# Optimization experiments

Hardware: AMD Instinct MI355X
Metric: run time of the kernel (lower is better)

Reference implementation:

```python
import jax, jax.numpy as jnp
import numpy as np

H = 128   # hidden_size
NL = 3    # num_layers
R = 32    # water_rows (Water2sea_slice_num)
O = 48    # water_cols (Original_slice_len)
B = 64    # batch_size
F = 32    # input_size
L = R + O - 1  # Water2sea_slice_len (wavefront length)


def setup_inputs():
    key = jax.random.key(0)
    k1, k2, k3, k4 = jax.random.split(key, 4)
    stdv = 1.0 / np.sqrt(H)
    inp = jax.random.normal(k1, (B, R, O, F), dtype=jnp.float32)
    W_first = jax.random.uniform(k2, (6 * H, F + 2 * H), minval=-stdv, maxval=stdv, dtype=jnp.float32)
    W_other = jax.random.uniform(k3, (NL - 1, 6 * H, 4 * H), minval=-stdv, maxval=stdv, dtype=jnp.float32)
    Bias = jax.random.uniform(k4, (NL, 6 * H), minval=-stdv, maxval=stdv, dtype=jnp.float32)
    return {"input": inp, "W_first": W_first, "W_other": W_other, "Bias": Bias,
            "batch_size": B, "input_size": F, "flag": 0}


def _forward(inp, W_first, W_other, Bias, batch_size, input_size, flag):
    # permute: flag==0 -> [rows, batch, cols, feat]
    x = jnp.transpose(inp, (2, 0, 1, 3)) if flag == 1 else jnp.transpose(inp, (1, 0, 2, 3))
    Rn, bs, On, Fn = x.shape
    Ln = Rn + On - 1
    # wavefront-shifted input: row r occupies slices [r, r+On) (input_transfer)
    padded = jnp.pad(x, ((0, 0), (0, 0), (0, Rn - 1), (0, 0)))                 # [R,B,L,F]
    shifted = jax.vmap(lambda t, r: jnp.roll(t, r, axis=1))(padded, jnp.arange(Rn))
    a0 = shifted.reshape(Rn * bs, Ln, Fn)
    # bias applied to row-group g at slice s iff (s < Rn) and (g <= s)  [faithful to linear()]
    s_idx = jnp.arange(Ln)[:, None]
    g_idx = jnp.arange(Rn)[None, :]
    bias_mask = ((g_idx <= s_idx) & (s_idx < Rn)).astype(jnp.float32)          # [L,R]
    bias_mask = jnp.repeat(bias_mask, bs, axis=1)[..., None]                   # [L,RB,1]

    def run_layer(a, W, bvec):
        # a: [RB, L, feat]; W: [6H, feat+2H]; bvec: [6H]
        def step(carry, xs):
            h_row, h_col = carry
            a_s, m_s = xs
            z = jnp.concatenate([h_row, h_col, a_s], axis=-1)
            gate = z @ W.T + m_s * bvec                                        # [RB,6H]
            sig = jax.nn.sigmoid(gate[:, :4 * H])
            tnh = jnp.tanh(gate[:, 4 * H:])
            ur, orow, uc, ocol = jnp.split(sig, 4, axis=-1)
            ir, ic = jnp.split(tnh, 2, axis=-1)
            h_row_n = jnp.tanh((1.0 - ur) * h_row + ur * ir) * orow
            h_col_n = jnp.tanh((1.0 - uc) * h_col + uc * ic) * ocol
            out = jnp.concatenate([h_row_n, h_col_n], axis=-1)
            h_col_roll = jnp.roll(h_col_n, bs, axis=0)  # transfer col hidden to next row
            return (h_row_n, h_col_roll), (out, h_row_n, h_col_n)
        h0 = jnp.zeros((Rn * bs, H), a.dtype)
        _, (outs, hrows, hcols) = jax.lax.scan(step, (h0, h0), (jnp.swapaxes(a, 0, 1), bias_mask))
        return outs, hrows, hcols  # each [L, RB, *]

    row_saves, col_saves = [], []
    a = a0
    for layer in range(NL):
        W = W_first if layer == 0 else W_other[layer - 1]
        outs, hrows, hcols = run_layer(a, W, Bias[layer])
        hrows = hrows.reshape(Ln, Rn, bs, H)
        hcols = hcols.reshape(Ln, Rn, bs, H)
        # row r finishes at slice On-1+r; col hidden of last row-group saved for slices >= Rn-1
        row_saves.append(hrows[On - 1 + jnp.arange(Rn), jnp.arange(Rn)])       # [R,B,H]
        col_saves.append(hcols[Rn - 1:, Rn - 1])                               # [O,B,H]
        a = jnp.swapaxes(outs, 0, 1)                                           # [RB,L,2H]; dropout p=0 -> identity
    output_all_slice = a
    hidden_row_all = jnp.transpose(jnp.stack(row_saves), (2, 0, 1, 3))         # [B,NL,R,H]
    hidden_col_all = jnp.transpose(jnp.stack(col_saves), (2, 0, 1, 3))         # [B,NL,O,H]
    return output_all_slice, hidden_row_all, hidden_col_all


def reference(input, W_first, W_other, Bias, batch_size, input_size, flag):
    return _forward(input, W_first, W_other, Bias, batch_size, input_size, flag)
```

## Files before the change

### kernel.cpp

```cpp
#include <hip/hip_runtime.h>
#include <stdint.h>

#define HH   128
#define NLAY 3
#define RR   32
#define OO   48
#define BBX  64
#define FFX  32
#define LLX  (RR + OO - 1)
#define RBr  (RR * BBX)
#define N6   (6 * HH)
#define TSTEPS (LLX + NLAY - 1)
#define NBLOCKS 192

typedef unsigned short u16;
typedef __attribute__((ext_vector_type(8))) short short8;
typedef __attribute__((ext_vector_type(4))) float f32x4;

#define OFF_ABUF0 ((size_t)0)
#define SZ_ABUF0  ((size_t)LLX * RBr * FFX * 2)
#define OFF_HZ    (OFF_ABUF0 + SZ_ABUF0)
#define SZ_HZ     ((size_t)NLAY * 2 * RBr * 256 * 2)
#define OFF_BAR   (OFF_HZ + SZ_HZ)
#define SZ_BAR    ((size_t)32768)
#define SZ_STATE  (SZ_HZ + SZ_BAR)

__device__ __forceinline__ u16 f2b(float x) {
  uint32_t u = __float_as_uint(x);
  return (u16)((u + 0x7FFFu + ((u >> 16) & 1u)) >> 16);
}
__device__ __forceinline__ float rcp_(float x) { return __builtin_amdgcn_rcpf(x); }
__device__ __forceinline__ float sigmoidf_(float x) {
  return rcp_(1.0f + __expf(-x));
}
__device__ __forceinline__ float tanhf_(float x) {
  return 1.0f - 2.0f * rcp_(__expf(2.0f * x) + 1.0f);
}

__global__ __launch_bounds__(256) void k_prep_input(const float* __restrict__ inp,
                                                    u16* __restrict__ abuf0) {
  int idx = blockIdx.x * 256 + threadIdx.x;
  if (idx >= LLX * RBr * FFX) return;
  int f   = idx & (FFX - 1);
  int row = (idx >> 5) & (RBr - 1);
  int s   = idx / (RBr * FFX);
  int g = row >> 6, b = row & 63;
  int o = s - g;
  float v = (o >= 0 && o < OO) ? inp[((b * RR + g) * OO + o) * FFX + f] : 0.0f;
  abuf0[idx] = f2b(v);
}

__global__ __launch_bounds__(256) void k_zero(uint32_t* __restrict__ p, size_t nwords) {
  size_t i = (size_t)blockIdx.x * 256 + threadIdx.x;
  size_t stride = (size_t)gridDim.x * 256;
  for (; i < nwords; i += stride) p[i] = 0u;
}

template <int KK>
__device__ __forceinline__ void stage_w(const float* __restrict__ Wsrc, int jblk,
                                        u16* __restrict__ Wl) {
  constexpr int NFRAG = (KK / 32) * 6;
  for (int e = threadIdx.x; e < NFRAG * 64; e += 1024) {
    int kcm = e >> 6, ln = e & 63;
    int kc = kcm / 6, m = kcm - kc * 6;
    int fr2 = ln & 15, hi2 = ln >> 4;
    int srow = m * 128 + jblk * 16 + fr2;
    const float* src = Wsrc + (size_t)srow * KK + kc * 32 + hi2 * 8;
    short8 v;
#pragma unroll
    for (int x = 0; x < 8; ++x) v[x] = (short)f2b(src[x]);
    *(short8*)&Wl[(size_t)e * 8] = v;
  }
}

template <int KK>
__device__ __forceinline__ void persist_body(char* __restrict__ ws,
                                             const float* __restrict__ Bias_l,
                                             float* __restrict__ out,
                                             int layer, int jblk, int bblk, bool light,
                                             u16* __restrict__ Wl,
                                             float* __restrict__ hcl,
                                             uint32_t* __restrict__ arrC,
                                             uint32_t* __restrict__ epoC,
                                             bool leader) {
  constexpr int NCH = KK / 32;
  constexpr int RD  = 6;
  const int tid = threadIdx.x;
  const int lane = tid & 63, w = tid >> 6;
  const int fr = lane & 15, hi = lane >> 4;
  const int myslot = layer * 8 + jblk;

  const int g0   = w * 2 + (fr >> 3);
  const int bcol = bblk * 8 + (fr & 7);
  const int arow = g0 * 64 + bcol;
  const int arp  = ((g0 + 1) & 31) * 64 + bcol;
  const int j = jblk * 16 + fr;
  const u16* wfrag = &Wl[lane * 8];
  float bia[6];
#pragma unroll
  for (int m = 0; m < 6; ++m) bia[m] = Bias_l[m * 128 + j];

  u16*   hz_base  = (u16*)(ws + OFF_HZ) + (size_t)layer * 2 * RBr * 256;
  u16*   hzp_base = (u16*)(ws + OFF_HZ) + (size_t)(layer - 1) * 2 * RBr * 256;
  u16*   abuf0    = (u16*)(ws + OFF_ABUF0);
  float* hid_row  = out + (size_t)RBr * LLX * 256;
  float* hid_col  = hid_row + (size_t)BBX * NLAY * RR * HH;

  float hr_reg[4];
#pragma unroll
  for (int q = 0; q < 4; ++q) hr_reg[q] = 0.0f;

  for (int t = 0; t < TSTEPS; ++t) {
    const int s = t - layer;
    const uint32_t target = (uint32_t)(t + 1);
    float sv_r[4], sv_c[4];
#pragma unroll
    for (int q = 0; q < 4; ++q) { sv_r[q] = 0.0f; sv_c[q] = 0.0f; }

    if (s >= 0 && s < LLX) {
      const int sW = s & 1, sR = sW ^ 1;
      const u16* hzR = hz_base + (size_t)sR * RBr * 256;
      u16*       hzW = hz_base + (size_t)sW * RBr * 256;
      const u16* hzP = hzp_base + (size_t)sW * RBr * 256;
      const u16* ab_s = abuf0 + (size_t)s * RBr * FFX;
      const float* hcR = hcl + sR * 4352;
      float*       hcW = hcl + sW * 4352;

      if (w * 2 <= s) {
        auto LDK = [&](int kc) -> short8 {
          if (kc < 8)
            return *(const short8*)&hzR[arow * 256 + kc * 32 + hi * 8];
          if constexpr (KK == 288) {
            return *(const short8*)&ab_s[arow * FFX + hi * 8];
          } else {
            if (kc < 12)
              return *(const short8*)&hzP[arow * 256 + (kc - 8) * 32 + hi * 8];
            return *(const short8*)&hzP[arp * 256 + 128 + (kc - 12) * 32 + hi * 8];
          }
        };

        f32x4 z4 = {0.f, 0.f, 0.f, 0.f};
        f32x4 acc[6];
#pragma unroll
        for (int m = 0; m < 6; ++m) acc[m] = z4;

        short8 ring[RD];
#pragma unroll
        for (int i = 0; i < RD && i < NCH; ++i) ring[i] = LDK(i);
        __builtin_amdgcn_s_setprio(1);
#pragma unroll
        for (int kc = 0; kc < NCH; ++kc) {
          short8 a = ring[kc % RD];
          if (kc + RD < NCH) ring[kc % RD] = LDK(kc + RD);
#pragma unroll
          for (int m = 0; m < 6; ++m) {
            short8 bv = *(const short8*)&wfrag[(size_t)(kc * 6 + m) * 512];
            acc[m] = __builtin_amdgcn_mfma_f32_16x16x32_bf16(a, bv, acc[m], 0, 0, 0);
          }
        }
        __builtin_amdgcn_s_setprio(0);

        const int g = w * 2 + (hi >> 1);
        const int gp = (g + 1) & (RR - 1);
        const float msk = (g <= s && s < RR) ? 1.0f : 0.0f;
        float mb[6];
#pragma unroll
        for (int m = 0; m < 6; ++m) mb[m] = msk * bia[m];
#pragma unroll
        for (int q = 0; q < 4; ++q) {
          const int lb = (hi & 1) * 4 + q;
          const int b  = bblk * 8 + lb;
          const int row = g * 64 + b;
          const int lrow = g * 8 + lb;
          const int rp = gp * 64 + b;
          const int lrp = gp * 8 + lb;
          float ur  = sigmoidf_(acc[0][q] + mb[0]);
          float orw = sigmoidf_(acc[1][q] + mb[1]);
          float uc  = sigmoidf_(acc[2][q] + mb[2]);
          float oc  = sigmoidf_(acc[3][q] + mb[3]);
          float ir  = tanhf_(acc[4][q] + mb[4]);
          float ic  = tanhf_(acc[5][q] + mb[5]);
          float hr_o = hr_reg[q];
          float hc_o = hcR[lrow * 17 + fr];
          float hr_n = tanhf_((1.0f - ur) * hr_o + ur * ir) * orw;
          float hc_n = tanhf_((1.0f - uc) * hc_o + uc * ic) * oc;
          hr_reg[q] = hr_n;
          sv_r[q] = hr_n;
          sv_c[q] = hc_n;
          hcW[lrp * 17 + fr] = hc_n;
          hzW[row * 256 + j] = f2b(hr_n);
          hzW[rp * 256 + HH + j] = f2b(hc_n);
        }
      } else {
        const int g = w * 2 + (hi >> 1);
        const int gp = (g + 1) & (RR - 1);
#pragma unroll
        for (int q = 0; q < 4; ++q) {
          const int lb = (hi & 1) * 4 + q;
          const int b  = bblk * 8 + lb;
          const int row = g * 64 + b;
          const int rp = gp * 64 + b;
          const int lrp = gp * 8 + lb;
          hcW[lrp * 17 + fr] = 0.0f;
          hzW[row * 256 + j] = 0;
          hzW[rp * 256 + HH + j] = 0;
        }
      }
    }

    __syncthreads();
    if (tid == 0) {
      if (!light) __threadfence();
      __hip_atomic_store(&arrC[myslot * 16], target, __ATOMIC_RELAXED,
                         __HIP_MEMORY_SCOPE_AGENT);
    }

    if (s >= 0 && s < LLX) {
      const int g = w * 2 + (hi >> 1);
#pragma unroll
      for (int q = 0; q < 4; ++q) {
        const int lb = (hi & 1) * 4 + q;
        const int b  = bblk * 8 + lb;
        const int row = g * 64 + b;
        if (layer == 2) {
          out[((size_t)row * LLX + s) * 256 + j] = sv_r[q];
          out[((size_t)row * LLX + s) * 256 + HH + j] = sv_c[q];
        }
        if (s - g == OO - 1)
          hid_row[((size_t)(b * NLAY + layer) * RR + g) * HH + j] = sv_r[q];
        if (g == RR - 1 && s >= RR - 1)
          hid_col[((size_t)(b * NLAY + layer) * OO + (s - (RR - 1))) * HH + j] = sv_c[q];
      }
    }

    if (leader) {
      if (tid < 24) {
        while (__hip_atomic_load(&arrC[tid * 16], __ATOMIC_RELAXED,
                                 __HIP_MEMORY_SCOPE_AGENT) < target)
          __builtin_amdgcn_s_sleep(1);
      }
      __syncthreads();
      if (tid == 0)
        __hip_atomic_store(epoC, target, __ATOMIC_RELAXED, __HIP_MEMORY_SCOPE_AGENT);
    }
    if (tid == 0) {
      while (__hip_atomic_load(epoC, __ATOMIC_RELAXED, __HIP_MEMORY_SCOPE_AGENT) < target)
        __builtin_amdgcn_s_sleep(1);
      if (!light) __threadfence();
    }
    __syncthreads();
    if (light) asm volatile("buffer_inv" ::: "memory");
  }
}

__global__ __launch_bounds__(1024, 4) void k_persist(char* __restrict__ ws,
                                                     const float* __restrict__ Wf,
                                                     const float* __restrict__ Wo,
                                                     const float* __restrict__ Bias,
                                                     float* __restrict__ out) {
  __shared__ u16 Wl[49152];
  __shared__ float hcl[8704];
  __shared__ uint32_t sh_light;
  const int bx = blockIdx.x;
  const int layer = bx >> 6, jblk = (bx >> 3) & 7, bblk = bx & 7;
  const int tid = threadIdx.x;

  if (layer == 0) stage_w<288>(Wf, jblk, Wl);
  else            stage_w<512>(Wo + (size_t)(layer - 1) * N6 * 512, jblk, Wl);
  for (int e = tid; e < 8704; e += 1024) hcl[e] = 0.0f;

  uint32_t xcc;
  asm volatile("s_getreg_b32 %0, hwreg(20, 0, 4)" : "=s"(xcc));
  uint32_t* barG  = (uint32_t*)(ws + OFF_BAR);
  uint32_t* table = (uint32_t*)(ws + OFF_BAR + 256);
  uint32_t* arrC  = (uint32_t*)(ws + OFF_BAR + 4096 + (size_t)bblk * 2048);
  uint32_t* epoC  = (uint32_t*)(ws + OFF_BAR + 24576 + (size_t)bblk * 256);
  const bool leader = (layer == 0 && jblk == 0);
  __syncthreads();
  if (tid == 0) {
    __hip_atomic_store(&table[bx], xcc, __ATOMIC_RELAXED, __HIP_MEMORY_SCOPE_AGENT);
    __hip_atomic_fetch_add(barG, 1u, __ATOMIC_RELEASE, __HIP_MEMORY_SCOPE_AGENT);
    while (__hip_atomic_load(barG, __ATOMIC_ACQUIRE, __HIP_MEMORY_SCOPE_AGENT) < NBLOCKS)
      __builtin_amdgcn_s_sleep(1);
    uint32_t lt = 1u;
    for (int q2 = 0; q2 < 24; ++q2) {
      uint32_t v = __hip_atomic_load(&table[q2 * 8 + bblk], __ATOMIC_RELAXED,
                                     __HIP_MEMORY_SCOPE_AGENT);
      lt &= (v == xcc) ? 1u : 0u;
    }
    sh_light = lt;
  }
  __syncthreads();
  const bool light = (sh_light != 0u);

  const float* bias_l = Bias + layer * N6;
  if (layer == 0)
    persist_body<288>(ws, bias_l, out, 0, jblk, bblk, light, Wl, hcl,
                      arrC, epoC, leader);
  else
    persist_body<512>(ws, bias_l, out, layer, jblk, bblk, light, Wl, hcl,
                      arrC, epoC, leader);
}

extern "C" void kernel_launch(void* const* d_in, const int* in_sizes, int n_in,
                              void* d_out, int out_size, void* d_ws, size_t ws_size,
                              hipStream_t stream) {
  const float* inp  = (const float*)d_in[0];
  const float* Wf   = (const float*)d_in[1];
  const float* Wo   = (const float*)d_in[2];
  const float* Bias = (const float*)d_in[3];
  float* out = (float*)d_out;
  char* ws = (char*)d_ws;
  (void)in_sizes; (void)n_in; (void)out_size; (void)ws_size;

  k_prep_input<<<(LLX * RBr * FFX) / 256, 256, 0, stream>>>(inp, (u16*)(ws + OFF_ABUF0));
  k_zero<<<2048, 256, 0, stream>>>((uint32_t*)(ws + OFF_HZ), SZ_STATE / 4);
  k_persist<<<NBLOCKS, 1024, 0, stream>>>(ws, Wf, Wo, Bias, out);
}
```

Measured before the change: 730.2 us.

## Halve block threads and give each wave two row-group tiles sharing weight fragments

Each block of the persistent kernel now runs 512 threads (8 waves) instead of 1024, and each wave handles two 16-row MFMA tiles. The weight fragment loaded from LDS is reused for both accumulator sets, which halves LDS weight reads per MFMA. The prefetch ring depth is cut to 3 per tile to limit register pressure, and the launch bound drops the min-blocks hint. The risks are fewer waves to hide latency, higher VGPR use, and an active-wave cutoff (w*4<=s) that is coarser at early slices, so some waves do extra MFMA work early on.

```diff
diff --git a/kernel.cpp b/kernel.cpp
--- a/kernel.cpp
+++ b/kernel.cpp
@@ -60,7 +60,7 @@
 __device__ __forceinline__ void stage_w(const float* __restrict__ Wsrc, int jblk,
                                         u16* __restrict__ Wl) {
   constexpr int NFRAG = (KK / 32) * 6;
-  for (int e = threadIdx.x; e < NFRAG * 64; e += 1024) {
+  for (int e = threadIdx.x; e < NFRAG * 64; e += 512) {
     int kcm = e >> 6, ln = e & 63;
     int kc = kcm / 6, m = kcm - kc * 6;
     int fr2 = ln & 15, hi2 = ln >> 4;
@@ -84,16 +84,19 @@
                                              uint32_t* __restrict__ epoC,
                                              bool leader) {
   constexpr int NCH = KK / 32;
-  constexpr int RD  = 6;
+  constexpr int RD  = 3;
   const int tid = threadIdx.x;
   const int lane = tid & 63, w = tid >> 6;
   const int fr = lane & 15, hi = lane >> 4;
   const int myslot = layer * 8 + jblk;
 
-  const int g0   = w * 2 + (fr >> 3);
   const int bcol = bblk * 8 + (fr & 7);
-  const int arow = g0 * 64 + bcol;
-  const int arp  = ((g0 + 1) & 31) * 64 + bcol;
+  const int g00   = w * 4 + (fr >> 3);
+  const int arow0 = g00 * 64 + bcol;
+  const int arp0  = ((g00 + 1) & 31) * 64 + bcol;
+  const int g01   = g00 + 2;
+  const int arow1 = g01 * 64 + bcol;
+  const int arp1  = ((g01 + 1) & 31) * 64 + bcol;
   const int j = jblk * 16 + fr;
   const u16* wfrag = &Wl[lane * 8];
   float bia[6];
@@ -106,16 +109,20 @@
   float* hid_row  = out + (size_t)RBr * LLX * 256;
   float* hid_col  = hid_row + (size_t)BBX * NLAY * RR * HH;
 
-  float hr_reg[4];
-#pragma unroll
-  for (int q = 0; q < 4; ++q) hr_reg[q] = 0.0f;
+  float hr_reg[2][4];
+#pragma unroll
+  for (int t2 = 0; t2 < 2; ++t2)
+#pragma unroll
+    for (int q = 0; q < 4; ++q) hr_reg[t2][q] = 0.0f;
 
   for (int t = 0; t < TSTEPS; ++t) {
     const int s = t - layer;
     const uint32_t target = (uint32_t)(t + 1);
-    float sv_r[4], sv_c[4];
-#pragma unroll
-    for (int q = 0; q < 4; ++q) { sv_r[q] = 0.0f; sv_c[q] = 0.0f; }
+    float sv_r[2][4], sv_c[2][4];
+#pragma unroll
+    for (int t2 = 0; t2 < 2; ++t2)
+#pragma unroll
+      for (int q = 0; q < 4; ++q) { sv_r[t2][q] = 0.0f; sv_c[t2][q] = 0.0f; }
 
     if (s >= 0 && s < LLX) {
       const int sW = s & 1, sR = sW ^ 1;
@@ -126,84 +133,99 @@
       const float* hcR = hcl + sR * 4352;
       float*       hcW = hcl + sW * 4352;
 
-      if (w * 2 <= s) {
-        auto LDK = [&](int kc) -> short8 {
+      if (w * 4 <= s) {
+        auto LDK = [&](int ar, int ap, int kc) -> short8 {
           if (kc < 8)
-            return *(const short8*)&hzR[arow * 256 + kc * 32 + hi * 8];
+            return *(const short8*)&hzR[ar * 256 + kc * 32 + hi * 8];
           if constexpr (KK == 288) {
-            return *(const short8*)&ab_s[arow * FFX + hi * 8];
+            return *(const short8*)&ab_s[ar * FFX + hi * 8];
           } else {
             if (kc < 12)
-              return *(const short8*)&hzP[arow * 256 + (kc - 8) * 32 + hi * 8];
-            return *(const short8*)&hzP[arp * 256 + 128 + (kc - 12) * 32 + hi * 8];
+              return *(const short8*)&hzP[ar * 256 + (kc - 8) * 32 + hi * 8];
+            return *(const short8*)&hzP[ap * 256 + 128 + (kc - 12) * 32 + hi * 8];
           }
         };
 
         f32x4 z4 = {0.f, 0.f, 0.f, 0.f};
-        f32x4 acc[6];
-#pragma unroll
-        for (int m = 0; m < 6; ++m) acc[m] = z4;
-
-        short8 ring[RD];
-#pragma unroll
-        for (int i = 0; i < RD && i < NCH; ++i) ring[i] = LDK(i);
+        f32x4 acc0[6], acc1[6];
+#pragma unroll
+        for (int m = 0; m < 6; ++m) { acc0[m] = z4; acc1[m] = z4; }
+
+        short8 ring0[RD], ring1[RD];
+#pragma unroll
+        for (int i = 0; i < RD; ++i) {
+          ring0[i] = LDK(arow0, arp0, i);
+          ring1[i] = LDK(arow1, arp1, i);
+        }
         __builtin_amdgcn_s_setprio(1);
 #pragma unroll
         for (int kc = 0; kc < NCH; ++kc) {
-          short8 a = ring[kc % RD];
-          if (kc + RD < NCH) ring[kc % RD] = LDK(kc + RD);
+          short8 a0 = ring0[kc % RD];
+          short8 a1 = ring1[kc % RD];
+          if (kc + RD < NCH) {
+            ring0[kc % RD] = LDK(arow0, arp0, kc + RD);
+            ring1[kc % RD] = LDK(arow1, arp1, kc + RD);
+          }
 #pragma unroll
           for (int m = 0; m < 6; ++m) {
             short8 bv = *(const short8*)&wfrag[(size_t)(kc * 6 + m) * 512];
-            acc[m] = __builtin_amdgcn_mfma_f32_16x16x32_bf16(a, bv, acc[m], 0, 0, 0);
+            acc0[m] = __builtin_amdgcn_mfma_f32_16x16x32_bf16(a0, bv, acc0[m], 0, 0, 0);
+            acc1[m] = __builtin_amdgcn_mfma_f32_16x16x32_bf16(a1, bv, acc1[m], 0, 0, 0);
           }
         }
         __builtin_amdgcn_s_setprio(0);
 
-        const int g = w * 2 + (hi >> 1);
-        const int gp = (g + 1) & (RR - 1);
-        const float msk = (g <= s && s < RR) ? 1.0f : 0.0f;
-        float mb[6];
-#pragma unroll
-        for (int m = 0; m < 6; ++m) mb[m] = msk * bia[m];
-#pragma unroll
-        for (int q = 0; q < 4; ++q) {
-          const int lb = (hi & 1) * 4 + q;
-          const int b  = bblk * 8 + lb;
-          const int row = g * 64 + b;
-          const int lrow = g * 8 + lb;
-          const int rp = gp * 64 + b;
-          const int lrp = gp * 8 + lb;
-          float ur  = sigmoidf_(acc[0][q] + mb[0]);
-          float orw = sigmoidf_(acc[1][q] + mb[1]);
-          float uc  = sigmoidf_(acc[2][q] + mb[2]);
-          float oc  = sigmoidf_(acc[3][q] + mb[3]);
-          float ir  = tanhf_(acc[4][q] + mb[4]);
-          float ic  = tanhf_(acc[5][q] + mb[5]);
-          float hr_o = hr_reg[q];
-          float hc_o = hcR[lrow * 17 + fr];
-          float hr_n = tanhf_((1.0f - ur) * hr_o + ur * ir) * orw;
-          float hc_n = tanhf_((1.0f - uc) * hc_o + uc * ic) * oc;
-          hr_reg[q] = hr_n;
-          sv_r[q] = hr_n;
-          sv_c[q] = hc_n;
-          hcW[lrp * 17 + fr] = hc_n;
-          hzW[row * 256 + j] = f2b(hr_n);
-          hzW[rp * 256 + HH + j] = f2b(hc_n);
+#pragma unroll
+        for (int t2 = 0; t2 < 2; ++t2) {
+          const int g = w * 4 + 2 * t2 + (hi >> 1);
+          const int gp = (g + 1) & (RR - 1);
+          const float msk = (g <= s && s < RR) ? 1.0f : 0.0f;
+          float mb[6];
+#pragma unroll
+          for (int m = 0; m < 6; ++m) mb[m] = msk * bia[m];
+#pragma unroll
+          for (int q = 0; q < 4; ++q) {
+            const f32x4* A = t2 ? acc1 : acc0;
+            const int lb = (hi & 1) * 4 + q;
+            const int b  = bblk * 8 + lb;
+            const int row = g * 64 + b;
+            const int lrow = g * 8 + lb;
+            const int rp = gp * 64 + b;
+            const int lrp = gp * 8 + lb;
+            float ur  = sigmoidf_(A[0][q] + mb[0]);
+            float orw = sigmoidf_(A[1][q] + mb[1]);
+            float uc  = sigmoidf_(A[2][q] + mb[2]);
+            float oc  = sigmoidf_(A[3][q] + mb[3]);
+            float ir  = tanhf_(A[4][q] + mb[4]);
+            float ic  = tanhf_(A[5][q] + mb[5]);
+            float hr_o = hr_reg[t2][q];
+            float hc_o = hcR[lrow * 17 + fr];
+            float hr_n = tanhf_((1.0f - ur) * hr_o + ur * ir) * orw;
+            float hc_n = tanhf_((1.0f - uc) * hc_o + uc * ic) * oc;
+            hr_reg[t2][q] = hr_n;
+            sv_r[t2][q] = hr_n;
+            sv_c[t2][q] = hc_n;
+            hcW[lrp * 17 + fr] = hc_n;
+            hzW[row * 256 + j] = f2b(hr_n);
+            hzW[rp * 256 + HH + j] = f2b(hc_n);
+          }
         }
       } else {
-        const int g = w * 2 + (hi >> 1);
-        const int gp = (g + 1) & (RR - 1);
-#pragma unroll
-        for (int q = 0; q < 4; ++q) {
-          const int lb = (hi & 1) * 4 + q;
-          const int b  = bblk * 8 + lb;
-          const int row = g * 64 + b;
-          const int rp = gp * 64 + b;
-          const int lrp = gp * 8 + lb;
-          hcW[lrp * 17 + fr] = 0.0f;
-          hzW[row * 256 + j] = 0;
-          hzW[rp * 256 + HH + j] = 0;
+#pragma unroll
+        for (int t2 = 0; t2 < 2; ++t2) {
+          const int g = w * 4 + 2 * t2 + (hi >> 1);
+          const int gp = (g + 1) & (RR - 1);
+#pragma unroll
+          for (int q = 0; q < 4; ++q) {
+            const int lb = (hi & 1) * 4 + q;
+            const int b  = bblk * 8 + lb;
+            const int row = g * 64 + b;
+            const int rp = gp * 64 + b;
+            const int lrp = gp * 8 + lb;
+            hcW[lrp * 17 + fr] = 0.0f;
+            hzW[row * 256 + j] = 0;
+            hzW[rp * 256 + HH + j] = 0;
+          }
         }
       }
     }
@@ -216,20 +238,23 @@
     }
 
     if (s >= 0 && s < LLX) {
-      const int g = w * 2 + (hi >> 1);
-#pragma unroll
-      for (int q = 0; q < 4; ++q) {
-        const int lb = (hi & 1) * 4 + q;
-        const int b  = bblk * 8 + lb;
-        const int row = g * 64 + b;
-        if (layer == 2) {
-          out[((size_t)row * LLX + s) * 256 + j] = sv_r[q];
-          out[((size_t)row * LLX + s) * 256 + HH + j] = sv_c[q];
-        }
-        if (s - g == OO - 1)
-          hid_row[((size_t)(b * NLAY + layer) * RR + g) * HH + j] = sv_r[q];
-        if (g == RR - 1 && s >= RR - 1)
-          hid_col[((size_t)(b * NLAY + layer) * OO + (s - (RR - 1))) * HH + j] = sv_c[q];
+#pragma unroll
+      for (int t2 = 0; t2 < 2; ++t2) {
+        const int g = w * 4 + 2 * t2 + (hi >> 1);
+#pragma unroll
+        for (int q = 0; q < 4; ++q) {
+          const int lb = (hi & 1) * 4 + q;
+          const int b  = bblk * 8 + lb;
+          const int row = g * 64 + b;
+          if (layer == 2) {
+            out[((size_t)row * LLX + s) * 256 + j] = sv_r[t2][q];
+            out[((size_t)row * LLX + s) * 256 + HH + j] = sv_c[t2][q];
+          }
+          if (s - g == OO - 1)
+            hid_row[((size_t)(b * NLAY + layer) * RR + g) * HH + j] = sv_r[t2][q];
+          if (g == RR - 1 && s >= RR - 1)
+            hid_col[((size_t)(b * NLAY + layer) * OO + (s - (RR - 1))) * HH + j] = sv_c[t2][q];
+        }
       }
     }
 
@@ -253,11 +278,11 @@
   }
 }
 
-__global__ __launch_bounds__(1024, 4) void k_persist(char* __restrict__ ws,
-                                                     const float* __restrict__ Wf,
-                                                     const float* __restrict__ Wo,
-                                                     const float* __restrict__ Bias,
-                                                     float* __restrict__ out) {
+__global__ __launch_bounds__(512) void k_persist(char* __restrict__ ws,
+                                                 const float* __restrict__ Wf,
+                                                 const float* __restrict__ Wo,
+                                                 const float* __restrict__ Bias,
+                                                 float* __restrict__ out) {
   __shared__ u16 Wl[49152];
   __shared__ float hcl[8704];
   __shared__ uint32_t sh_light;
@@ -267,7 +292,7 @@
 
   if (layer == 0) stage_w<288>(Wf, jblk, Wl);
   else            stage_w<512>(Wo + (size_t)(layer - 1) * N6 * 512, jblk, Wl);
-  for (int e = tid; e < 8704; e += 1024) hcl[e] = 0.0f;
+  for (int e = tid; e < 8704; e += 512) hcl[e] = 0.0f;
 
   uint32_t xcc;
   asm volatile("s_getreg_b32 %0, hwreg(20, 0, 4)" : "=s"(xcc));
@@ -315,5 +340,5 @@
 
   k_prep_input<<<(LLX * RBr * FFX) / 256, 256, 0, stream>>>(inp, (u16*)(ws + OFF_ABUF0));
   k_zero<<<2048, 256, 0, stream>>>((uint32_t*)(ws + OFF_HZ), SZ_STATE / 4);
-  k_persist<<<NBLOCKS, 1024, 0, stream>>>(ws, Wf, Wo, Bias, out);
-}
+  k_persist<<<NBLOCKS, 512, 0, stream>>>(ws, Wf, Wo, Bias, out);
+}
```

Measured after the change: 789.1 us. 1.08x slower.

## Shrink LDS weight tile by streaming tail weight fragments from global memory

Applied to the files above, without the earlier changes.

Layers 1-2 now keep only the first 64 weight fragments per block in shared memory. The remaining 32 fragments are prepacked to bf16 in a workspace buffer by a new prep kernel and streamed from global/L2 through a 12-deep register ring during the MFMA loop. This cuts LDS from 96KB to 64KB for the weight tile, presumably to ease LDS pressure or allow better residency. The cost is extra global loads on the latency-critical recurrent step and more register use.

```diff
diff --git a/kernel.cpp b/kernel.cpp
--- a/kernel.cpp
+++ b/kernel.cpp
@@ -24,6 +24,8 @@
 #define OFF_BAR   (OFF_HZ + SZ_HZ)
 #define SZ_BAR    ((size_t)32768)
 #define SZ_STATE  (SZ_HZ + SZ_BAR)
+#define OFF_WG    (OFF_BAR + SZ_BAR)
+#define SZ_WG     ((size_t)2 * 8 * 32 * 512 * 2)
 
 __device__ __forceinline__ u16 f2b(float x) {
   uint32_t u = __float_as_uint(x);
@@ -50,6 +52,24 @@
   abuf0[idx] = f2b(v);
 }
 
+__global__ __launch_bounds__(256) void k_prep_wg(const float* __restrict__ Wo,
+                                                 u16* __restrict__ Wg) {
+  int idx = blockIdx.x * 256 + threadIdx.x;
+  if (idx >= 2 * 8 * 32 * 64) return;
+  int lane = idx & 63;
+  int fg   = (idx >> 6) & 31;
+  int jb   = (idx >> 11) & 7;
+  int l2   = idx >> 14;
+  int kcm = 64 + fg;
+  int kc = kcm / 6, m = kcm - kc * 6;
+  int fr = lane & 15, hi = lane >> 4;
+  int srow = m * 128 + jb * 16 + fr;
+  const float* src = Wo + (size_t)l2 * N6 * 512 + (size_t)srow * 512 + kc * 32 + hi * 8;
+  u16* dst = Wg + ((size_t)((l2 * 8 + jb) * 32 + fg)) * 512 + lane * 8;
+#pragma unroll
+  for (int x = 0; x < 8; ++x) dst[x] = f2b(src[x]);
+}
+
 __global__ __launch_bounds__(256) void k_zero(uint32_t* __restrict__ p, size_t nwords) {
   size_t i = (size_t)blockIdx.x * 256 + threadIdx.x;
   size_t stride = (size_t)gridDim.x * 256;
@@ -59,7 +79,7 @@
 template <int KK>
 __device__ __forceinline__ void stage_w(const float* __restrict__ Wsrc, int jblk,
                                         u16* __restrict__ Wl) {
-  constexpr int NFRAG = (KK / 32) * 6;
+  constexpr int NFRAG = (KK == 512) ? 64 : (KK / 32) * 6;
   for (int e = threadIdx.x; e < NFRAG * 64; e += 1024) {
     int kcm = e >> 6, ln = e & 63;
     int kc = kcm / 6, m = kcm - kc * 6;
@@ -96,6 +116,8 @@
   const int arp  = ((g0 + 1) & 31) * 64 + bcol;
   const int j = jblk * 16 + fr;
   const u16* wfrag = &Wl[lane * 8];
+  const u16* wg = (u16*)(ws + OFF_WG) +
+                  ((size_t)((layer - 1) * 8 + jblk)) * 32 * 512 + lane * 8;
   float bia[6];
 #pragma unroll
   for (int m = 0; m < 6; ++m) bia[m] = Bias_l[m * 128 + j];
@@ -147,6 +169,13 @@
         short8 ring[RD];
 #pragma unroll
         for (int i = 0; i < RD && i < NCH; ++i) ring[i] = LDK(i);
+
+        short8 wring[12];
+        if constexpr (KK == 512) {
+#pragma unroll
+          for (int i = 0; i < 12; ++i) wring[i] = *(const short8*)(wg + i * 512);
+        }
+
         __builtin_amdgcn_s_setprio(1);
 #pragma unroll
         for (int kc = 0; kc < NCH; ++kc) {
@@ -154,7 +183,20 @@
           if (kc + RD < NCH) ring[kc % RD] = LDK(kc + RD);
 #pragma unroll
           for (int m = 0; m < 6; ++m) {
-            short8 bv = *(const short8*)&wfrag[(size_t)(kc * 6 + m) * 512];
+            const int kcm = kc * 6 + m;
+            short8 bv;
+            if constexpr (KK == 512) {
+              if (kcm < 64) {
+                bv = *(const short8*)&wfrag[(size_t)kcm * 512];
+              } else {
+                const int fg = kcm - 64;
+                bv = wring[fg % 12];
+                if (fg + 12 < 32)
+                  wring[fg % 12] = *(const short8*)(wg + (fg + 12) * 512);
+              }
+            } else {
+              bv = *(const short8*)&wfrag[(size_t)kcm * 512];
+            }
             acc[m] = __builtin_amdgcn_mfma_f32_16x16x32_bf16(a, bv, acc[m], 0, 0, 0);
           }
         }
@@ -258,7 +300,7 @@
                                                      const float* __restrict__ Wo,
                                                      const float* __restrict__ Bias,
                                                      float* __restrict__ out) {
-  __shared__ u16 Wl[49152];
+  __shared__ u16 Wl[64 * 512];
   __shared__ float hcl[8704];
   __shared__ uint32_t sh_light;
   const int bx = blockIdx.x;
@@ -314,6 +356,7 @@
   (void)in_sizes; (void)n_in; (void)out_size; (void)ws_size;
 
   k_prep_input<<<(LLX * RBr * FFX) / 256, 256, 0, stream>>>(inp, (u16*)(ws + OFF_ABUF0));
+  k_prep_wg<<<128, 256, 0, stream>>>(Wo, (u16*)(ws + OFF_WG));
   k_zero<<<2048, 256, 0, stream>>>((uint32_t*)(ws + OFF_HZ), SZ_STATE / 4);
   k_persist<<<NBLOCKS, 1024, 0, stream>>>(ws, Wf, Wo, Bias, out);
 }
```

After: 1.813 ms. 2.48x slower.
